# Kernel optimization log

Measured on AMD Instinct MI355X. Metric: run time of the kernel, lower is better.

The kernel has to match this reference:

```python
import jax, jax.numpy as jnp
import numpy as np

EMBED = 768
HIDDEN = 4 * EMBED
TEMPERATURE = 1.0
LN_EPS = 1e-5


def setup_inputs() -> dict:
    key = jax.random.key(0)
    ks = jax.random.split(key, 10)
    s = 1.0 / np.sqrt(EMBED)
    sh = 1.0 / np.sqrt(HIDDEN)
    return {
        "x": jax.random.normal(ks[0], (32, 577, EMBED), dtype=jnp.float32),
        "Wq": jax.random.normal(ks[1], (EMBED, EMBED), dtype=jnp.float32) * s,
        "Wk": jax.random.normal(ks[2], (EMBED, EMBED), dtype=jnp.float32) * s,
        "Wv": jax.random.normal(ks[3], (EMBED, EMBED), dtype=jnp.float32) * s,
        "ln1_g": jnp.ones((EMBED,), jnp.float32),
        "ln1_b": jnp.zeros((EMBED,), jnp.float32),
        "ln2_g": jnp.ones((EMBED,), jnp.float32),
        "ln2_b": jnp.zeros((EMBED,), jnp.float32),
        "W1": jax.random.normal(ks[4], (EMBED, HIDDEN), dtype=jnp.float32) * s,
        "b1": jnp.zeros((HIDDEN,), jnp.float32),
        "W2": jax.random.normal(ks[5], (HIDDEN, EMBED), dtype=jnp.float32) * sh,
        "b2": jnp.zeros((EMBED,), jnp.float32),
    }


def layer_norm(x, g, b):
    mu = jnp.mean(x, axis=-1, keepdims=True)
    var = jnp.mean(jnp.square(x - mu), axis=-1, keepdims=True)
    return (x - mu) * jax.lax.rsqrt(var + LN_EPS) * g + b


def l2_attention(h, Wq, Wk, Wv):
    # h: [b, s, d]
    Q = h @ Wq
    K = h @ Wk
    V = h @ Wv
    q_sq = jnp.sum(Q * Q, axis=-1, keepdims=True)          # [b, s, 1]
    k_sq = jnp.sum(K * K, axis=-1, keepdims=True)          # [b, s, 1]
    qk = jnp.einsum('bqd,bkd->bqk', Q, K)                  # [b, s, s]
    l2_sq = q_sq + jnp.swapaxes(k_sq, -2, -1) - 2.0 * qk
    attn = jax.nn.softmax(-l2_sq / TEMPERATURE, axis=-1)
    return jnp.einsum('bqk,bkd->bqd', attn, V)


def reference(x, Wq, Wk, Wv, ln1_g, ln1_b, ln2_g, ln2_b, W1, b1, W2, b2):
    x = x + l2_attention(layer_norm(x, ln1_g, ln1_b), Wq, Wk, Wv)
    h = layer_norm(x, ln2_g, ln2_b)
    h = jax.nn.gelu(h @ W1 + b1, approximate=False) @ W2 + b2
    return x + h
```

## Files before the change

### kernel.cpp

```cpp
#include <hip/hip_runtime.h>

#define EMBED 768
#define HIDDEN 3072
#define SEQ 577
#define BATCH 32
#define ROWS (BATCH*SEQ)
#define KPAD 608
#define SLD 640

typedef __attribute__((ext_vector_type(4))) float f32x4;
typedef __attribute__((ext_vector_type(8))) __bf16 bf16x8;
typedef unsigned int __attribute__((address_space(1))) as1_u32;
typedef unsigned int __attribute__((address_space(3))) as3_u32;

__device__ __forceinline__ unsigned short f2b(float f) {
    unsigned int u = __float_as_uint(f);
    u = u + 0x7FFFu + ((u >> 16) & 1u);
    return (unsigned short)(u >> 16);
}
__device__ __forceinline__ float b2f(unsigned short s) {
    return __uint_as_float(((unsigned int)s) << 16);
}
__device__ __forceinline__ void gld16(const unsigned short* g, unsigned short* l) {
    __builtin_amdgcn_global_load_lds((const as1_u32*)g, (as3_u32*)l, 16, 0, 0);
}
__device__ __forceinline__ float gelu_f(float x) {
    float u = x * (0.7978845608028654f + 0.03567740814183f * x * x);
    float e = __expf(2.0f * u);
    float th = 1.0f - 2.0f / (e + 1.0f);
    return 0.5f * x * (1.0f + th);
}

__device__ __forceinline__ int swz_lin() {
    int nx = gridDim.x;
    int lin = blockIdx.y * nx + blockIdx.x;
    if (gridDim.z == 1) {
        int nwg = nx * gridDim.y;
        int q = nwg >> 3, r = nwg & 7;
        int xcd = lin & 7, blk = lin >> 3;
        lin = (xcd < r ? xcd * (q + 1) : r * (q + 1) + (xcd - r) * q) + blk;
    }
    return lin;
}

__global__ void ln_kernel(const float* __restrict__ x, const float* __restrict__ g,
                          const float* __restrict__ b, unsigned short* __restrict__ o) {
    int row = blockIdx.x;
    const float* xr = x + (size_t)row * EMBED;
    int t = threadIdx.x;
    float v0 = xr[t], v1 = xr[t + 256], v2 = xr[t + 512];
    float s = v0 + v1 + v2;
    float ss = v0 * v0 + v1 * v1 + v2 * v2;
#pragma unroll
    for (int d = 32; d; d >>= 1) { s += __shfl_down(s, d); ss += __shfl_down(ss, d); }
    __shared__ float rs[4], rss[4];
    if ((t & 63) == 0) { rs[t >> 6] = s; rss[t >> 6] = ss; }
    __syncthreads();
    s = rs[0] + rs[1] + rs[2] + rs[3];
    ss = rss[0] + rss[1] + rss[2] + rss[3];
    float mu = s * (1.0f / EMBED);
    float var = ss * (1.0f / EMBED) - mu * mu;
    float rstd = rsqrtf(var + 1e-5f);
    unsigned short* orow = o + (size_t)row * EMBED;
    orow[t]       = f2b((v0 - mu) * rstd * g[t]       + b[t]);
    orow[t + 256] = f2b((v1 - mu) * rstd * g[t + 256] + b[t + 256]);
    orow[t + 512] = f2b((v2 - mu) * rstd * g[t + 512] + b[t + 512]);
}

__global__ void ln_split_kernel(const float* __restrict__ x, const float* __restrict__ g,
                                const float* __restrict__ b, unsigned short* __restrict__ oh,
                                unsigned short* __restrict__ ol) {
    int row = blockIdx.x;
    const float* xr = x + (size_t)row * EMBED;
    int t = threadIdx.x;
    float v0 = xr[t], v1 = xr[t + 256], v2 = xr[t + 512];
    float s = v0 + v1 + v2;
    float ss = v0 * v0 + v1 * v1 + v2 * v2;
#pragma unroll
    for (int d = 32; d; d >>= 1) { s += __shfl_down(s, d); ss += __shfl_down(ss, d); }
    __shared__ float rs[4], rss[4];
    if ((t & 63) == 0) { rs[t >> 6] = s; rss[t >> 6] = ss; }
    __syncthreads();
    s = rs[0] + rs[1] + rs[2] + rs[3];
    ss = rss[0] + rss[1] + rss[2] + rss[3];
    float mu = s * (1.0f / EMBED);
    float var = ss * (1.0f / EMBED) - mu * mu;
    float rstd = rsqrtf(var + 1e-5f);
    size_t base = (size_t)row * EMBED;
#pragma unroll
    for (int i = 0; i < 3; i++) {
        int d = t + 256 * i;
        float v = (i == 0 ? v0 : (i == 1 ? v1 : v2));
        float y = (v - mu) * rstd * g[d] + b[d];
        unsigned short h = f2b(y);
        oh[base + d] = h;
        ol[base + d] = f2b(y - b2f(h));
    }
}

__global__ void ksq_kernel(const unsigned short* __restrict__ qh,
                           const unsigned short* __restrict__ ql, float* __restrict__ ksq) {
    int row = blockIdx.x;
    int t = threadIdx.x;
    size_t base = (size_t)row * 1536 + EMBED;
    float s = 0.f;
#pragma unroll
    for (int i = 0; i < 3; i++) {
        int d = t + 256 * i;
        float k = b2f(qh[base + d]) + b2f(ql[base + d]);
        s += k * k;
    }
#pragma unroll
    for (int d = 32; d; d >>= 1) s += __shfl_down(s, d);
    __shared__ float rs[4];
    if ((t & 63) == 0) rs[t >> 6] = s;
    __syncthreads();
    if (t == 0) ksq[row] = rs[0] + rs[1] + rs[2] + rs[3];
}

__global__ void softmax_kernel(const float* __restrict__ S, unsigned short* __restrict__ P) {
    int r = blockIdx.x;
    int t = threadIdx.x;
    const float* sr = S + (size_t)r * SLD;
    float v0 = sr[t];
    float v1 = sr[t + 256];
    float v2 = (t + 512 < SEQ) ? sr[t + 512] : -3.0e38f;
    float m = fmaxf(v0, fmaxf(v1, v2));
#pragma unroll
    for (int d = 32; d; d >>= 1) m = fmaxf(m, __shfl_down(m, d));
    __shared__ float rm[4];
    if ((t & 63) == 0) rm[t >> 6] = m;
    __syncthreads();
    m = fmaxf(fmaxf(rm[0], rm[1]), fmaxf(rm[2], rm[3]));
    float e0 = __expf(v0 - m);
    float e1 = __expf(v1 - m);
    float e2 = (t + 512 < SEQ) ? __expf(v2 - m) : 0.0f;
    float s = e0 + e1 + e2;
#pragma unroll
    for (int d = 32; d; d >>= 1) s += __shfl_down(s, d);
    __shared__ float rsum[4];
    if ((t & 63) == 0) rsum[t >> 6] = s;
    __syncthreads();
    float inv = 1.0f / (rsum[0] + rsum[1] + rsum[2] + rsum[3]);
    unsigned short* pr = P + (size_t)r * KPAD;
    pr[t]       = f2b(e0 * inv);
    pr[t + 256] = f2b(e1 * inv);
    if (t + 512 < KPAD) pr[t + 512] = f2b(e2 * inv);
}

__global__ void wt_kernel(const float* __restrict__ in, unsigned short* __restrict__ out,
                          int K, int N, int outRowOff, int outLd) {
    __shared__ float tile[32][33];
    int n0 = blockIdx.x * 32, k0 = blockIdx.y * 32;
    int tx = threadIdx.x, ty = threadIdx.y;
#pragma unroll
    for (int i = 0; i < 4; i++)
        tile[ty + 8 * i][tx] = in[(size_t)(k0 + ty + 8 * i) * N + (n0 + tx)];
    __syncthreads();
#pragma unroll
    for (int i = 0; i < 4; i++)
        out[(size_t)(outRowOff + n0 + ty + 8 * i) * outLd + (k0 + tx)] = f2b(tile[tx][ty + 8 * i]);
}

__global__ void wt_split2_kernel(const float* __restrict__ Wq, const float* __restrict__ Wk,
                                 unsigned short* __restrict__ oh, unsigned short* __restrict__ ol) {
    const float* in = blockIdx.z ? Wk : Wq;
    int outRowOff = blockIdx.z * EMBED;
    __shared__ float tile[32][33];
    int n0 = blockIdx.x * 32, k0 = blockIdx.y * 32;
    int tx = threadIdx.x, ty = threadIdx.y;
#pragma unroll
    for (int i = 0; i < 4; i++)
        tile[ty + 8 * i][tx] = in[(size_t)(k0 + ty + 8 * i) * EMBED + (n0 + tx)];
    __syncthreads();
#pragma unroll
    for (int i = 0; i < 4; i++) {
        float v = tile[tx][ty + 8 * i];
        unsigned short h = f2b(v);
        size_t idx = (size_t)(outRowOff + n0 + ty + 8 * i) * EMBED + (k0 + tx);
        oh[idx] = h;
        ol[idx] = f2b(v - b2f(h));
    }
}

__global__ void vt_kernel(const unsigned short* __restrict__ vbuf, unsigned short* __restrict__ vt) {
    int z = blockIdx.z;
    int d0 = blockIdx.x * 32, c0 = blockIdx.y * 32;
    __shared__ unsigned short tile[32][33];
    int tx = threadIdx.x, ty = threadIdx.y;
#pragma unroll
    for (int i = 0; i < 4; i++) {
        int c = c0 + ty + 8 * i;
        tile[ty + 8 * i][tx] = (c < SEQ) ? vbuf[((size_t)z * SEQ + c) * EMBED + d0 + tx]
                                         : (unsigned short)0;
    }
    __syncthreads();
#pragma unroll
    for (int i = 0; i < 4; i++) {
        int d = d0 + 8 * i + ty, c = c0 + tx;
        vt[(size_t)z * EMBED * KPAD + (size_t)d * KPAD + c] = tile[tx][ty + 8 * i];
    }
}

template <int EPI>
__global__ __launch_bounds__(512, 4) void gemm_bt(
    const unsigned short* __restrict__ A, int lda, long long sA,
    const unsigned short* __restrict__ B, int ldb, long long sB,
    int M, int N, int K,
    void* __restrict__ C, int ldc, long long sC,
    const float* __restrict__ E, long long sE) {
    __shared__ unsigned short As[3][8192];
    __shared__ unsigned short Bs[3][4096];
    int z = blockIdx.z;
    A += (size_t)z * sA;
    B += (size_t)z * sB;
    int nx = gridDim.x;
    int lin = swz_lin();
    int row0 = (lin / nx) * 256, col0 = (lin % nx) * 128;
    int t = threadIdx.x, l = t & 63, w = t >> 6;
    int wr = w >> 1, wc = w & 1;
    int l15 = l & 15, kb = l >> 4;

    f32x4 acc[4][4] = {};

    int srow = t >> 2;
    int kboff = ((t & 3) ^ ((srow >> 1) & 3)) * 8;

    int aoE[2], boE;
#pragma unroll
    for (int c = 0; c < 2; ++c) {
        int ar = row0 + c * 128 + srow; ar = ar < M ? ar : M - 1;
        aoE[c] = ar * lda + kboff;
    }
    {
        int br = col0 + srow; br = br < N ? br : N - 1;
        boE = br * ldb + kboff;
    }
    int aoff[4], boff[4];
#pragma unroll
    for (int m = 0; m < 4; m++) {
        int r = wr * 64 + m * 16 + l15;
        aoff[m] = r * 32 + (kb ^ ((r >> 1) & 3)) * 8;
        int rn = wc * 64 + m * 16 + l15;
        boff[m] = rn * 32 + (kb ^ ((rn >> 1) & 3)) * 8;
    }

    auto compute = [&](int sl) {
        bf16x8 af[4], bfr[4];
#pragma unroll
        for (int m = 0; m < 4; m++) af[m] = *reinterpret_cast<const bf16x8*>(&As[sl][aoff[m]]);
#pragma unroll
        for (int n = 0; n < 4; n++) bfr[n] = *reinterpret_cast<const bf16x8*>(&Bs[sl][boff[n]]);
#pragma unroll
        for (int m = 0; m < 4; m++)
#pragma unroll
            for (int n = 0; n < 4; n++)
                acc[m][n] = __builtin_amdgcn_mfma_f32_16x16x32_bf16(af[m], bfr[n], acc[m][n], 0, 0, 0);
    };

    int ldsoff = t * 8;
    for (int kt = 0; kt < K; kt += 96) {
#pragma unroll
        for (int s = 0; s < 3; ++s) {
            int ks = kt + 32 * s;
            if (ks < K) {
                gld16(A + (size_t)(aoE[0] + ks), &As[s][ldsoff]);
                gld16(A + (size_t)(aoE[1] + ks), &As[s][4096 + ldsoff]);
                gld16(B + (size_t)(boE + ks), &Bs[s][ldsoff]);
            }
        }
        asm volatile("s_waitcnt vmcnt(0)" ::: "memory");
        __builtin_amdgcn_s_barrier();
        __builtin_amdgcn_sched_barrier(0);
#pragma unroll
        for (int s = 0; s < 3; ++s)
            if (kt + 32 * s < K) compute(s);
        __builtin_amdgcn_s_barrier();
        __builtin_amdgcn_sched_barrier(0);
    }

    int rbase = row0 + wr * 64 + (l >> 4) * 4;
    int cbase = col0 + wc * 64 + l15;
    auto epi = [&](bool chk) {
#pragma unroll
        for (int m = 0; m < 4; m++) {
#pragma unroll
            for (int n = 0; n < 4; n++) {
                int col = cbase + n * 16;
                if (chk && col >= N) continue;
#pragma unroll
                for (int j = 0; j < 4; j++) {
                    int row = rbase + m * 16 + j;
                    if (chk && row >= M) continue;
                    float v = acc[m][n][j];
                    size_t oidx = (size_t)z * sC + (size_t)row * ldc + col;
                    if (EPI == 0) {
                        ((unsigned short*)C)[oidx] = f2b(v);
                    } else if (EPI == 2) {
                        ((float*)C)[oidx] = E[oidx] + v;
                    } else if (EPI == 3) {
                        ((unsigned short*)C)[oidx] = f2b(gelu_f(v + E[col]));
                    } else if (EPI == 4) {
                        ((float*)C)[oidx] += v + E[col];
                    }
                }
            }
        }
    };
    if (row0 + 256 <= M && col0 + 128 <= N) epi(false); else epi(true);
}

template <int EPI>
__global__ __launch_bounds__(512, 2) void gemm_hp(
    const unsigned short* __restrict__ Ah, const unsigned short* __restrict__ Al, int lda, long long sA,
    const unsigned short* __restrict__ Bh, const unsigned short* __restrict__ Bl, int ldb, long long sB,
    int M, int N, int K,
    void* __restrict__ C, int ldc, long long sC, long long planeOff,
    const float* __restrict__ E, long long sE) {
    __shared__ unsigned short Ash[8192], Asl[8192], Bsh[4096], Bsl[4096];
    int z = blockIdx.z;
    Ah += (size_t)z * sA; Al += (size_t)z * sA;
    Bh += (size_t)z * sB; Bl += (size_t)z * sB;
    int nx = gridDim.x;
    int lin = swz_lin();
    int row0 = (lin / nx) * 256, col0 = (lin % nx) * 128;
    int t = threadIdx.x, l = t & 63, w = t >> 6;
    int wr = w >> 1, wc = w & 1;
    int l15 = l & 15, kb = l >> 4;

    f32x4 acc[4][4] = {};

    int srow = t >> 2;
    int kboff = ((t & 3) ^ ((srow >> 1) & 3)) * 8;

    int aoE[2], boE;
#pragma unroll
    for (int c = 0; c < 2; ++c) {
        int ar = row0 + c * 128 + srow; ar = ar < M ? ar : M - 1;
        aoE[c] = ar * lda + kboff;
    }
    {
        int br = col0 + srow; br = br < N ? br : N - 1;
        boE = br * ldb + kboff;
    }
    int aoff[4], boff[4];
#pragma unroll
    for (int m = 0; m < 4; m++) {
        int r = wr * 64 + m * 16 + l15;
        aoff[m] = r * 32 + (kb ^ ((r >> 1) & 3)) * 8;
        int rn = wc * 64 + m * 16 + l15;
        boff[m] = rn * 32 + (kb ^ ((rn >> 1) & 3)) * 8;
    }

    int ldsoff = t * 8;
    for (int kt = 0; kt < K; kt += 32) {
        gld16(Ah + (size_t)(aoE[0] + kt), &Ash[ldsoff]);
        gld16(Ah + (size_t)(aoE[1] + kt), &Ash[4096 + ldsoff]);
        gld16(Al + (size_t)(aoE[0] + kt), &Asl[ldsoff]);
        gld16(Al + (size_t)(aoE[1] + kt), &Asl[4096 + ldsoff]);
        gld16(Bh + (size_t)(boE + kt), &Bsh[ldsoff]);
        gld16(Bl + (size_t)(boE + kt), &Bsl[ldsoff]);
        __syncthreads();
        bf16x8 afh[4], afl[4], bfh[4], bfl[4];
#pragma unroll
        for (int m = 0; m < 4; m++) {
            afh[m] = *reinterpret_cast<const bf16x8*>(&Ash[aoff[m]]);
            afl[m] = *reinterpret_cast<const bf16x8*>(&Asl[aoff[m]]);
        }
#pragma unroll
        for (int n = 0; n < 4; n++) {
            bfh[n] = *reinterpret_cast<const bf16x8*>(&Bsh[boff[n]]);
            bfl[n] = *reinterpret_cast<const bf16x8*>(&Bsl[boff[n]]);
        }
#pragma unroll
        for (int m = 0; m < 4; m++)
#pragma unroll
            for (int n = 0; n < 4; n++) {
                acc[m][n] = __builtin_amdgcn_mfma_f32_16x16x32_bf16(afh[m], bfh[n], acc[m][n], 0, 0, 0);
                acc[m][n] = __builtin_amdgcn_mfma_f32_16x16x32_bf16(afh[m], bfl[n], acc[m][n], 0, 0, 0);
                acc[m][n] = __builtin_amdgcn_mfma_f32_16x16x32_bf16(afl[m], bfh[n], acc[m][n], 0, 0, 0);
            }
        __syncthreads();
    }

    int rbase = row0 + wr * 64 + (l >> 4) * 4;
    int cbase = col0 + wc * 64 + l15;
    auto epi = [&](bool chk) {
#pragma unroll
        for (int m = 0; m < 4; m++) {
#pragma unroll
            for (int n = 0; n < 4; n++) {
                int col = cbase + n * 16;
                if (chk && col >= N) continue;
#pragma unroll
                for (int j = 0; j < 4; j++) {
                    int row = rbase + m * 16 + j;
                    if (chk && row >= M) continue;
                    float v = acc[m][n][j];
                    size_t oidx = (size_t)z * sC + (size_t)row * ldc + col;
                    if (EPI == 0) {
                        unsigned short h = f2b(v);
                        ((unsigned short*)C)[oidx] = h;
                        ((unsigned short*)C)[oidx + planeOff] = f2b(v - b2f(h));
                    } else if (EPI == 1) {
                        ((float*)C)[oidx] = 2.0f * v - E[(size_t)z * sE + col];
                    }
                }
            }
        }
    };
    if (row0 + 256 <= M && col0 + 128 <= N) epi(false); else epi(true);
}

extern "C" void kernel_launch(void* const* d_in, const int* in_sizes, int n_in,
                              void* d_out, int out_size, void* d_ws, size_t ws_size,
                              hipStream_t stream) {
    const float* x   = (const float*)d_in[0];
    const float* Wq  = (const float*)d_in[1];
    const float* Wk  = (const float*)d_in[2];
    const float* Wv  = (const float*)d_in[3];
    const float* g1  = (const float*)d_in[4];
    const float* be1 = (const float*)d_in[5];
    const float* g2  = (const float*)d_in[6];
    const float* be2 = (const float*)d_in[7];
    const float* W1  = (const float*)d_in[8];
    const float* bb1 = (const float*)d_in[9];
    const float* W2  = (const float*)d_in[10];
    const float* bb2 = (const float*)d_in[11];
    float* out = (float*)d_out;

    char* ws = (char*)d_ws;
    size_t off = 0;
    auto alloc = [&](size_t bytes) -> char* {
        char* p = ws + off;
        off += (bytes + 255) & ~(size_t)255;
        return p;
    };
    unsigned short* wqkTh = (unsigned short*)alloc((size_t)1536 * EMBED * 2);
    unsigned short* wqkTl = (unsigned short*)alloc((size_t)1536 * EMBED * 2);
    unsigned short* wvT   = (unsigned short*)alloc((size_t)EMBED * EMBED * 2);
    unsigned short* w1T   = (unsigned short*)alloc((size_t)HIDDEN * EMBED * 2);
    unsigned short* w2T   = (unsigned short*)alloc((size_t)EMBED * HIDDEN * 2);
    float*          ksqb  = (float*)alloc((size_t)ROWS * 4);
    char* regB = alloc((size_t)ROWS * HIDDEN * 2);
    char* regC = alloc((size_t)2 * ROWS * EMBED * 2);
    unsigned short* vbuf  = (unsigned short*)alloc((size_t)ROWS * EMBED * 2);
    unsigned short* vtb   = (unsigned short*)alloc((size_t)BATCH * EMBED * KPAD * 2);
    unsigned short* Pbuf  = (unsigned short*)alloc((size_t)ROWS * KPAD * 2);
    if (off > ws_size) return;

    unsigned short* qkh  = (unsigned short*)regB;
    unsigned short* qkl  = qkh + (size_t)ROWS * 1536;
    unsigned short* hid  = (unsigned short*)regB;
    unsigned short* h1h  = (unsigned short*)regC;
    unsigned short* h1l  = h1h + (size_t)ROWS * EMBED;
    float*          Sbuf = (float*)regC;
    unsigned short* h2   = (unsigned short*)regC;

    dim3 b256(256), b512(512), bT(32, 8);

    wt_split2_kernel<<<dim3(24, 24, 2), bT, 0, stream>>>(Wq, Wk, wqkTh, wqkTl);
    wt_kernel<<<dim3(24, 24), bT, 0, stream>>>(Wv, wvT, EMBED, EMBED, 0, EMBED);
    wt_kernel<<<dim3(96, 24), bT, 0, stream>>>(W1, w1T, EMBED, HIDDEN, 0, EMBED);
    wt_kernel<<<dim3(24, 96), bT, 0, stream>>>(W2, w2T, HIDDEN, EMBED, 0, HIDDEN);

    ln_split_kernel<<<ROWS, b256, 0, stream>>>(x, g1, be1, h1h, h1l);

    gemm_hp<0><<<dim3(12, 73, 1), b512, 0, stream>>>(
        h1h, h1l, EMBED, 0, wqkTh, wqkTl, EMBED, 0,
        ROWS, 1536, EMBED, qkh, 1536, 0, (long long)ROWS * 1536, nullptr, 0);

    gemm_bt<0><<<dim3(6, 73, 1), b512, 0, stream>>>(
        h1h, EMBED, 0, wvT, EMBED, 0, ROWS, EMBED, EMBED, vbuf, EMBED, 0, nullptr, 0);

    ksq_kernel<<<ROWS, b256, 0, stream>>>(qkh, qkl, ksqb);

    gemm_hp<1><<<dim3(5, 3, 32), b512, 0, stream>>>(
        qkh, qkl, 1536, (long long)SEQ * 1536, qkh + EMBED, qkl + EMBED, 1536, (long long)SEQ * 1536,
        SEQ, SEQ, EMBED, Sbuf, SLD, (long long)SEQ * SLD, 0, ksqb, SEQ);

    softmax_kernel<<<ROWS, b256, 0, stream>>>(Sbuf, Pbuf);

    vt_kernel<<<dim3(24, 19, 32), bT, 0, stream>>>(vbuf, vtb);

    gemm_bt<2><<<dim3(6, 3, 32), b512, 0, stream>>>(
        Pbuf, KPAD, (long long)SEQ * KPAD, vtb, KPAD, (long long)EMBED * KPAD,
        SEQ, EMBED, KPAD, out, EMBED, (long long)SEQ * EMBED, x, (long long)SEQ * EMBED);

    ln_kernel<<<ROWS, b256, 0, stream>>>(out, g2, be2, h2);

    gemm_bt<3><<<dim3(24, 73, 1), b512, 0, stream>>>(
        h2, EMBED, 0, w1T, EMBED, 0, ROWS, HIDDEN, EMBED, hid, HIDDEN, 0, bb1, 0);

    gemm_bt<4><<<dim3(6, 73, 1), b512, 0, stream>>>(
        hid, HIDDEN, 0, w2T, HIDDEN, 0, ROWS, EMBED, HIDDEN, out, EMBED, 0, bb2, 0);
}
```

Measured before the change: 724.6 us.

## Fuse V transpose into V-projection epilogue and add 128x128 GEMM for FFN1

The V-projection GEMM now writes its output directly in the transposed, KPAD-padded layout through a new epilogue mode. This removes the separate vbuf buffer and the vt_kernel transpose pass. The first FFN GEMM switches to a new 256-thread 128x128-tile kernel with a simple two-stage load/compute loop, to raise block count and occupancy. Risks: the transposed epilogue does strided 2-byte stores and no longer zero-fills the padding columns of vtb. The new kernel also waits on all loads each iteration, so it does not overlap loads with compute.

```diff
diff --git a/kernel.cpp b/kernel.cpp
--- a/kernel.cpp
+++ b/kernel.cpp
@@ -183,27 +183,113 @@
     }
 }
 
-__global__ void vt_kernel(const unsigned short* __restrict__ vbuf, unsigned short* __restrict__ vt) {
+template <int EPI>
+__global__ __launch_bounds__(256, 2) void gemm_bt128(
+    const unsigned short* __restrict__ A, int lda, long long sA,
+    const unsigned short* __restrict__ B, int ldb, long long sB,
+    int M, int N, int K,
+    void* __restrict__ C, int ldc, long long sC,
+    const float* __restrict__ E, long long sE) {
+    __shared__ unsigned short As[2][4096];
+    __shared__ unsigned short Bs[2][4096];
     int z = blockIdx.z;
-    int d0 = blockIdx.x * 32, c0 = blockIdx.y * 32;
-    __shared__ unsigned short tile[32][33];
-    int tx = threadIdx.x, ty = threadIdx.y;
-#pragma unroll
-    for (int i = 0; i < 4; i++) {
-        int c = c0 + ty + 8 * i;
-        tile[ty + 8 * i][tx] = (c < SEQ) ? vbuf[((size_t)z * SEQ + c) * EMBED + d0 + tx]
-                                         : (unsigned short)0;
-    }
-    __syncthreads();
-#pragma unroll
-    for (int i = 0; i < 4; i++) {
-        int d = d0 + 8 * i + ty, c = c0 + tx;
-        vt[(size_t)z * EMBED * KPAD + (size_t)d * KPAD + c] = tile[tx][ty + 8 * i];
-    }
+    A += (size_t)z * sA;
+    B += (size_t)z * sB;
+    int nx = gridDim.x;
+    int lin = swz_lin();
+    int row0 = (lin / nx) * 128, col0 = (lin % nx) * 128;
+    int t = threadIdx.x, l = t & 63, w = t >> 6;
+    int wr = w >> 1, wc = w & 1;
+    int l15 = l & 15, kb = l >> 4;
+
+    f32x4 acc[4][4] = {};
+
+    int srow = t >> 2;
+    int kboff = ((t & 3) ^ ((srow >> 1) & 3)) * 8;
+
+    int aoE[2], boE[2];
+#pragma unroll
+    for (int c = 0; c < 2; ++c) {
+        int ar = row0 + c * 64 + srow; ar = ar < M ? ar : M - 1;
+        aoE[c] = ar * lda + kboff;
+        int br = col0 + c * 64 + srow; br = br < N ? br : N - 1;
+        boE[c] = br * ldb + kboff;
+    }
+    int aoff[4], boff[4];
+#pragma unroll
+    for (int m = 0; m < 4; m++) {
+        int r = wr * 64 + m * 16 + l15;
+        aoff[m] = r * 32 + (kb ^ ((r >> 1) & 3)) * 8;
+        int rn = wc * 64 + m * 16 + l15;
+        boff[m] = rn * 32 + (kb ^ ((rn >> 1) & 3)) * 8;
+    }
+
+    auto compute = [&](int sl) {
+        bf16x8 af[4], bfr[4];
+#pragma unroll
+        for (int m = 0; m < 4; m++) af[m] = *reinterpret_cast<const bf16x8*>(&As[sl][aoff[m]]);
+#pragma unroll
+        for (int n = 0; n < 4; n++) bfr[n] = *reinterpret_cast<const bf16x8*>(&Bs[sl][boff[n]]);
+#pragma unroll
+        for (int m = 0; m < 4; m++)
+#pragma unroll
+            for (int n = 0; n < 4; n++)
+                acc[m][n] = __builtin_amdgcn_mfma_f32_16x16x32_bf16(af[m], bfr[n], acc[m][n], 0, 0, 0);
+    };
+
+    int ldsoff = t * 8;
+    for (int kt = 0; kt < K; kt += 64) {
+        gld16(A + (size_t)(aoE[0] + kt), &As[0][ldsoff]);
+        gld16(A + (size_t)(aoE[1] + kt), &As[0][2048 + ldsoff]);
+        gld16(B + (size_t)(boE[0] + kt), &Bs[0][ldsoff]);
+        gld16(B + (size_t)(boE[1] + kt), &Bs[0][2048 + ldsoff]);
+        bool has2 = (kt + 32) < K;
+        if (has2) {
+            gld16(A + (size_t)(aoE[0] + kt + 32), &As[1][ldsoff]);
+            gld16(A + (size_t)(aoE[1] + kt + 32), &As[1][2048 + ldsoff]);
+            gld16(B + (size_t)(boE[0] + kt + 32), &Bs[1][ldsoff]);
+            gld16(B + (size_t)(boE[1] + kt + 32), &Bs[1][2048 + ldsoff]);
+        }
+        asm volatile("s_waitcnt vmcnt(0)" ::: "memory");
+        __builtin_amdgcn_s_barrier();
+        __builtin_amdgcn_sched_barrier(0);
+        compute(0);
+        if (has2) compute(1);
+        __builtin_amdgcn_s_barrier();
+        __builtin_amdgcn_sched_barrier(0);
+    }
+
+    int rbase = row0 + wr * 64 + (l >> 4) * 4;
+    int cbase = col0 + wc * 64 + l15;
+    auto epi = [&](bool chk) {
+#pragma unroll
+        for (int m = 0; m < 4; m++) {
+#pragma unroll
+            for (int n = 0; n < 4; n++) {
+                int col = cbase + n * 16;
+                if (chk && col >= N) continue;
+#pragma unroll
+                for (int j = 0; j < 4; j++) {
+                    int row = rbase + m * 16 + j;
+                    if (chk && row >= M) continue;
+                    float v = acc[m][n][j];
+                    size_t oidx = (size_t)z * sC + (size_t)row * ldc + col;
+                    if (EPI == 0) {
+                        ((unsigned short*)C)[oidx] = f2b(v);
+                    } else if (EPI == 3) {
+                        ((unsigned short*)C)[oidx] = f2b(gelu_f(v + E[col]));
+                    } else if (EPI == 4) {
+                        ((float*)C)[oidx] += v + E[col];
+                    }
+                }
+            }
+        }
+    };
+    if (row0 + 128 <= M && col0 + 128 <= N) epi(false); else epi(true);
 }
 
 template <int EPI>
-__global__ __launch_bounds__(512, 4) void gemm_bt(
+__global__ __launch_bounds__(512, 4) void gemm_bt256(
     const unsigned short* __restrict__ A, int lda, long long sA,
     const unsigned short* __restrict__ B, int ldb, long long sB,
     int M, int N, int K,
@@ -293,15 +379,17 @@
                     int row = rbase + m * 16 + j;
                     if (chk && row >= M) continue;
                     float v = acc[m][n][j];
-                    size_t oidx = (size_t)z * sC + (size_t)row * ldc + col;
-                    if (EPI == 0) {
-                        ((unsigned short*)C)[oidx] = f2b(v);
-                    } else if (EPI == 2) {
-                        ((float*)C)[oidx] = E[oidx] + v;
-                    } else if (EPI == 3) {
-                        ((unsigned short*)C)[oidx] = f2b(gelu_f(v + E[col]));
-                    } else if (EPI == 4) {
-                        ((float*)C)[oidx] += v + E[col];
+                    if (EPI == 5) {
+                        int zz = row / SEQ;
+                        int cc = row - zz * SEQ;
+                        ((unsigned short*)C)[(size_t)zz * (EMBED * KPAD) + (size_t)col * KPAD + cc] = f2b(v);
+                    } else {
+                        size_t oidx = (size_t)z * sC + (size_t)row * ldc + col;
+                        if (EPI == 2) {
+                            ((float*)C)[oidx] = E[oidx] + v;
+                        } else if (EPI == 4) {
+                            ((float*)C)[oidx] += v + E[col];
+                        }
                     }
                 }
             }
@@ -444,7 +532,6 @@
     float*          ksqb  = (float*)alloc((size_t)ROWS * 4);
     char* regB = alloc((size_t)ROWS * HIDDEN * 2);
     char* regC = alloc((size_t)2 * ROWS * EMBED * 2);
-    unsigned short* vbuf  = (unsigned short*)alloc((size_t)ROWS * EMBED * 2);
     unsigned short* vtb   = (unsigned short*)alloc((size_t)BATCH * EMBED * KPAD * 2);
     unsigned short* Pbuf  = (unsigned short*)alloc((size_t)ROWS * KPAD * 2);
     if (off > ws_size) return;
@@ -470,8 +557,8 @@
         h1h, h1l, EMBED, 0, wqkTh, wqkTl, EMBED, 0,
         ROWS, 1536, EMBED, qkh, 1536, 0, (long long)ROWS * 1536, nullptr, 0);
 
-    gemm_bt<0><<<dim3(6, 73, 1), b512, 0, stream>>>(
-        h1h, EMBED, 0, wvT, EMBED, 0, ROWS, EMBED, EMBED, vbuf, EMBED, 0, nullptr, 0);
+    gemm_bt256<5><<<dim3(6, 73, 1), b512, 0, stream>>>(
+        h1h, EMBED, 0, wvT, EMBED, 0, ROWS, EMBED, EMBED, vtb, 0, 0, nullptr, 0);
 
     ksq_kernel<<<ROWS, b256, 0, stream>>>(qkh, qkl, ksqb);
 
@@ -481,17 +568,15 @@
 
     softmax_kernel<<<ROWS, b256, 0, stream>>>(Sbuf, Pbuf);
 
-    vt_kernel<<<dim3(24, 19, 32), bT, 0, stream>>>(vbuf, vtb);
-
-    gemm_bt<2><<<dim3(6, 3, 32), b512, 0, stream>>>(
+    gemm_bt256<2><<<dim3(6, 3, 32), b512, 0, stream>>>(
         Pbuf, KPAD, (long long)SEQ * KPAD, vtb, KPAD, (long long)EMBED * KPAD,
         SEQ, EMBED, KPAD, out, EMBED, (long long)SEQ * EMBED, x, (long long)SEQ * EMBED);
 
     ln_kernel<<<ROWS, b256, 0, stream>>>(out, g2, be2, h2);
 
-    gemm_bt<3><<<dim3(24, 73, 1), b512, 0, stream>>>(
+    gemm_bt128<3><<<dim3(24, 145, 1), b256, 0, stream>>>(
         h2, EMBED, 0, w1T, EMBED, 0, ROWS, HIDDEN, EMBED, hid, HIDDEN, 0, bb1, 0);
 
-    gemm_bt<4><<<dim3(6, 73, 1), b512, 0, stream>>>(
+    gemm_bt256<4><<<dim3(6, 73, 1), b512, 0, stream>>>(
         hid, HIDDEN, 0, w2T, HIDDEN, 0, ROWS, EMBED, HIDDEN, out, EMBED, 0, bb2, 0);
 }
```

Result: no change. 727.6 us (+0.4%).

## Fuse K squared-norm into QK GEMM epilogue and use wave-per-row softmax

Applied to the files above, without the earlier changes.

Computes the squared norm of K rows inside the QK projection GEMM epilogue from the fp32 accumulators. Partial sums go per 128-column block via atomics into a small buffer, and a tiny kernel then sums the six partials. This removes a full pass re-reading the hi/lo K planes. Softmax is also rewritten so each 64-lane wave owns one row, using shuffle-xor reductions with no shared memory or barriers. The norm is now taken from unrounded fp32 values rather than the hi+lo reconstruction, and an extra memset plus atomics are added.

```diff
diff --git a/kernel.cpp b/kernel.cpp
--- a/kernel.cpp
+++ b/kernel.cpp
@@ -98,54 +98,45 @@
     }
 }
 
-__global__ void ksq_kernel(const unsigned short* __restrict__ qh,
-                           const unsigned short* __restrict__ ql, float* __restrict__ ksq) {
-    int row = blockIdx.x;
-    int t = threadIdx.x;
-    size_t base = (size_t)row * 1536 + EMBED;
+__global__ void ksq_reduce_kernel(const float* __restrict__ ksqp, float* __restrict__ ksqb) {
+    int row = blockIdx.x * 256 + threadIdx.x;
+    if (row >= ROWS) return;
+    const float* p = ksqp + (size_t)row * 8;
+    float s = p[0];
+    s += p[1]; s += p[2]; s += p[3]; s += p[4]; s += p[5];
+    ksqb[row] = s;
+}
+
+__global__ void softmax_kernel(const float* __restrict__ S, unsigned short* __restrict__ P) {
+    int r = blockIdx.x * 4 + (threadIdx.x >> 6);
+    int lane = threadIdx.x & 63;
+    const float* sr = S + (size_t)r * SLD;
+    float v[10];
+    float m = -3.0e38f;
+#pragma unroll
+    for (int i = 0; i < 10; i++) {
+        int c = lane + 64 * i;
+        v[i] = (c < SEQ) ? sr[c] : -3.0e38f;
+        m = fmaxf(m, v[i]);
+    }
+#pragma unroll
+    for (int d = 32; d; d >>= 1) m = fmaxf(m, __shfl_xor(m, d));
     float s = 0.f;
 #pragma unroll
-    for (int i = 0; i < 3; i++) {
-        int d = t + 256 * i;
-        float k = b2f(qh[base + d]) + b2f(ql[base + d]);
-        s += k * k;
-    }
-#pragma unroll
-    for (int d = 32; d; d >>= 1) s += __shfl_down(s, d);
-    __shared__ float rs[4];
-    if ((t & 63) == 0) rs[t >> 6] = s;
-    __syncthreads();
-    if (t == 0) ksq[row] = rs[0] + rs[1] + rs[2] + rs[3];
-}
-
-__global__ void softmax_kernel(const float* __restrict__ S, unsigned short* __restrict__ P) {
-    int r = blockIdx.x;
-    int t = threadIdx.x;
-    const float* sr = S + (size_t)r * SLD;
-    float v0 = sr[t];
-    float v1 = sr[t + 256];
-    float v2 = (t + 512 < SEQ) ? sr[t + 512] : -3.0e38f;
-    float m = fmaxf(v0, fmaxf(v1, v2));
-#pragma unroll
-    for (int d = 32; d; d >>= 1) m = fmaxf(m, __shfl_down(m, d));
-    __shared__ float rm[4];
-    if ((t & 63) == 0) rm[t >> 6] = m;
-    __syncthreads();
-    m = fmaxf(fmaxf(rm[0], rm[1]), fmaxf(rm[2], rm[3]));
-    float e0 = __expf(v0 - m);
-    float e1 = __expf(v1 - m);
-    float e2 = (t + 512 < SEQ) ? __expf(v2 - m) : 0.0f;
-    float s = e0 + e1 + e2;
-#pragma unroll
-    for (int d = 32; d; d >>= 1) s += __shfl_down(s, d);
-    __shared__ float rsum[4];
-    if ((t & 63) == 0) rsum[t >> 6] = s;
-    __syncthreads();
-    float inv = 1.0f / (rsum[0] + rsum[1] + rsum[2] + rsum[3]);
+    for (int i = 0; i < 10; i++) {
+        int c = lane + 64 * i;
+        v[i] = (c < SEQ) ? __expf(v[i] - m) : 0.0f;
+        s += v[i];
+    }
+#pragma unroll
+    for (int d = 32; d; d >>= 1) s += __shfl_xor(s, d);
+    float inv = 1.0f / s;
     unsigned short* pr = P + (size_t)r * KPAD;
-    pr[t]       = f2b(e0 * inv);
-    pr[t + 256] = f2b(e1 * inv);
-    if (t + 512 < KPAD) pr[t + 512] = f2b(e2 * inv);
+#pragma unroll
+    for (int i = 0; i < 10; i++) {
+        int c = lane + 64 * i;
+        if (c < KPAD) pr[c] = f2b(v[i] * inv);
+    }
 }
 
 __global__ void wt_kernel(const float* __restrict__ in, unsigned short* __restrict__ out,
@@ -316,7 +307,8 @@
     const unsigned short* __restrict__ Bh, const unsigned short* __restrict__ Bl, int ldb, long long sB,
     int M, int N, int K,
     void* __restrict__ C, int ldc, long long sC, long long planeOff,
-    const float* __restrict__ E, long long sE) {
+    const float* __restrict__ E, long long sE,
+    float* __restrict__ ksqp, int kqoff) {
     __shared__ unsigned short Ash[8192], Asl[8192], Bsh[4096], Bsl[4096];
     int z = blockIdx.z;
     Ah += (size_t)z * sA; Al += (size_t)z * sA;
@@ -410,6 +402,25 @@
         }
     };
     if (row0 + 256 <= M && col0 + 128 <= N) epi(false); else epi(true);
+
+    if (EPI == 0 && col0 >= kqoff) {
+        int cb = (col0 - kqoff) >> 7;
+#pragma unroll
+        for (int m = 0; m < 4; m++) {
+#pragma unroll
+            for (int j = 0; j < 4; j++) {
+                float s = 0.f;
+#pragma unroll
+                for (int n = 0; n < 4; n++) { float v = acc[m][n][j]; s += v * v; }
+                s += __shfl_xor(s, 1);
+                s += __shfl_xor(s, 2);
+                s += __shfl_xor(s, 4);
+                s += __shfl_xor(s, 8);
+                int row = rbase + m * 16 + j;
+                if (l15 == 0 && row < M) atomicAdd(&ksqp[(size_t)row * 8 + cb], s);
+            }
+        }
+    }
 }
 
 extern "C" void kernel_launch(void* const* d_in, const int* in_sizes, int n_in,
@@ -442,6 +453,7 @@
     unsigned short* w1T   = (unsigned short*)alloc((size_t)HIDDEN * EMBED * 2);
     unsigned short* w2T   = (unsigned short*)alloc((size_t)EMBED * HIDDEN * 2);
     float*          ksqb  = (float*)alloc((size_t)ROWS * 4);
+    float*          ksqp  = (float*)alloc((size_t)ROWS * 8 * 4);
     char* regB = alloc((size_t)ROWS * HIDDEN * 2);
     char* regC = alloc((size_t)2 * ROWS * EMBED * 2);
     unsigned short* vbuf  = (unsigned short*)alloc((size_t)ROWS * EMBED * 2);
@@ -459,6 +471,8 @@
 
     dim3 b256(256), b512(512), bT(32, 8);
 
+    hipMemsetAsync(ksqp, 0, (size_t)ROWS * 8 * 4, stream);
+
     wt_split2_kernel<<<dim3(24, 24, 2), bT, 0, stream>>>(Wq, Wk, wqkTh, wqkTl);
     wt_kernel<<<dim3(24, 24), bT, 0, stream>>>(Wv, wvT, EMBED, EMBED, 0, EMBED);
     wt_kernel<<<dim3(96, 24), bT, 0, stream>>>(W1, w1T, EMBED, HIDDEN, 0, EMBED);
@@ -468,18 +482,20 @@
 
     gemm_hp<0><<<dim3(12, 73, 1), b512, 0, stream>>>(
         h1h, h1l, EMBED, 0, wqkTh, wqkTl, EMBED, 0,
-        ROWS, 1536, EMBED, qkh, 1536, 0, (long long)ROWS * 1536, nullptr, 0);
+        ROWS, 1536, EMBED, qkh, 1536, 0, (long long)ROWS * 1536, nullptr, 0,
+        ksqp, EMBED);
 
     gemm_bt<0><<<dim3(6, 73, 1), b512, 0, stream>>>(
         h1h, EMBED, 0, wvT, EMBED, 0, ROWS, EMBED, EMBED, vbuf, EMBED, 0, nullptr, 0);
 
-    ksq_kernel<<<ROWS, b256, 0, stream>>>(qkh, qkl, ksqb);
+    ksq_reduce_kernel<<<(ROWS + 255) / 256, b256, 0, stream>>>(ksqp, ksqb);
 
     gemm_hp<1><<<dim3(5, 3, 32), b512, 0, stream>>>(
         qkh, qkl, 1536, (long long)SEQ * 1536, qkh + EMBED, qkl + EMBED, 1536, (long long)SEQ * 1536,
-        SEQ, SEQ, EMBED, Sbuf, SLD, (long long)SEQ * SLD, 0, ksqb, SEQ);
-
-    softmax_kernel<<<ROWS, b256, 0, stream>>>(Sbuf, Pbuf);
+        SEQ, SEQ, EMBED, Sbuf, SLD, (long long)SEQ * SLD, 0, ksqb, SEQ,
+        nullptr, 1 << 30);
+
+    softmax_kernel<<<ROWS / 4, b256, 0, stream>>>(Sbuf, Pbuf);
 
     vt_kernel<<<dim3(24, 19, 32), bT, 0, stream>>>(vbuf, vtb);
 
```

New measurement: 723.9 us. No clear change (-0.1%).
